# Kernel optimization log

Hardware: AMD Instinct MI355X
Metric: run time of the kernel (lower is better)

Reference implementation:

```python
import jax, jax.numpy as jnp
import numpy as np

HID = 128
OUT = 128
NC = 100000
NA = 1024
FC = 256
FA = 4096

def _sage(x_src, x_dst, ei, Wl, bl, Wr):
    # PyG SAGEConv, mean aggregation, bipartite:
    # out[i] = lin_l(mean_{j->i} x_src[j]) + lin_r(x_dst[i])
    n_dst = x_dst.shape[0]
    src, dst = ei[0], ei[1]
    msg = x_src[src]                                  # [E, F_src] gather
    agg = jax.ops.segment_sum(msg, dst, num_segments=n_dst)
    cnt = jax.ops.segment_sum(jnp.ones((ei.shape[1],), x_src.dtype), dst, num_segments=n_dst)
    mean = agg / jnp.clip(cnt, 1.0, None)[:, None]
    return mean @ Wl.T + bl + x_dst @ Wr.T

def setup_inputs() -> dict:
    key = jax.random.key(0)
    ks = jax.random.split(key, 20)
    d = {}
    d["article_x"] = jax.random.normal(ks[0], (1, FA), jnp.float32)
    d["community_x"] = jax.random.normal(ks[1], (NC, FC), jnp.float32)
    # bipartite edges: row = article node idx (<NA), col = community idx (<NC)
    d["e_wb"] = jnp.stack([jax.random.randint(ks[2], (500000,), 0, NA, jnp.int32),
                            jax.random.randint(ks[3], (500000,), 0, NC, jnp.int32)])
    d["e_mb"] = jnp.stack([jax.random.randint(ks[4], (500000,), 0, NA, jnp.int32),
                            jax.random.randint(ks[5], (500000,), 0, NC, jnp.int32)])
    d["e_cc"] = jax.random.randint(ks[6], (2, 800000), 0, NC, jnp.int32)
    s = lambda k, sh: jax.random.normal(k, sh, jnp.float32) * (1.0 / np.sqrt(sh[-1]))
    d["W_lin1"] = s(ks[7], (NA, FA)); d["b_lin1"] = jnp.zeros((NA,), jnp.float32)
    d["Wl1"] = s(ks[8], (HID, 1));   d["bl1"] = jnp.zeros((HID,), jnp.float32); d["Wr1"] = s(ks[9], (HID, FC))
    d["Wl2"] = s(ks[10], (HID, 1));  d["bl2"] = jnp.zeros((HID,), jnp.float32); d["Wr2"] = s(ks[11], (HID, HID))
    d["Wl3"] = s(ks[12], (HID, HID)); d["bl3"] = jnp.zeros((HID,), jnp.float32); d["Wr3"] = s(ks[13], (HID, FC))
    d["W_lin2"] = s(ks[14], (OUT, HID)); d["b_lin2"] = jnp.zeros((OUT,), jnp.float32)
    d["Wd1"] = s(ks[15], (OUT, 2 * OUT)); d["bd1"] = jnp.zeros((OUT,), jnp.float32)
    d["Wd2"] = s(ks[16], (1, OUT)); d["bd2"] = jnp.zeros((1,), jnp.float32)
    return d

def reference(article_x, community_x, e_wb, e_mb, e_cc,
              W_lin1, b_lin1, Wl1, bl1, Wr1, Wl2, bl2, Wr2,
              Wl3, bl3, Wr3, W_lin2, b_lin2, Wd1, bd1, Wd2, bd2):
    # encoder
    art = (article_x @ W_lin1.T + b_lin1).reshape(NA, 1)      # [1024, 1]
    h1 = jax.nn.relu(_sage(art, community_x, e_wb, Wl1, bl1, Wr1))   # [NC, HID]
    h2 = jax.nn.relu(_sage(art, h1, e_mb, Wl2, bl2, Wr2))            # [NC, HID]
    h3 = jax.nn.relu(_sage(h2, community_x, e_cc, Wl3, bl3, Wr3))    # [NC, HID]
    z = h3 @ W_lin2.T + b_lin2                                       # [NC, OUT]
    # edge decoder on interacts_with edges
    row, col = e_cc[0], e_cc[1]
    zz = jnp.concatenate([z[row], z[col]], axis=-1)                  # [E, 2*OUT]
    h = jax.nn.relu(zz @ Wd1.T + bd1)
    return (h @ Wd2.T + bd2).reshape(-1)                             # [E]
```

## Files before the change

kernel.cpp:

```cpp
#include <hip/hip_runtime.h>

#define NC 100000
#define NA 1024
#define FA 4096
#define MAXD 40

typedef _Float16 half8 __attribute__((ext_vector_type(8)));
typedef _Float16 half4v __attribute__((ext_vector_type(4)));
typedef _Float16 half2v __attribute__((ext_vector_type(2)));
typedef float floatx4 __attribute__((ext_vector_type(4)));

#define CNT_OFF 4294967296.0
#define CNT_INV 2.3283064365386963e-10

__device__ __forceinline__ void cvt_range(const float* __restrict__ in,
                                          _Float16* __restrict__ out, int n4,
                                          int bid, int nb) {
    int t = bid * 256 + threadIdx.x;
    int stride = nb * 256;
    for (int i = t; i < n4; i += stride) {
        float4 v = ((const float4*)in)[i];
        half4v h = {(_Float16)v.x, (_Float16)v.y, (_Float16)v.z, (_Float16)v.w};
        ((half4v*)out)[i] = h;
    }
}

__device__ __forceinline__ void edge_seg(const int* __restrict__ ei, int E,
                                         const float* __restrict__ art,
                                         double* __restrict__ acd, int bid, int nb) {
    int t = bid * 256 + threadIdx.x;
    int stride = nb * 256;
    for (int e = t; e < E; e += stride) {
        int s = ei[e], d = ei[E + e];
        atomicAdd(&acd[d], (double)art[s] + CNT_OFF);
    }
}

__device__ __forceinline__ void scat_seg(const int* __restrict__ ei, int E,
                                         int* __restrict__ cnt, int2* __restrict__ se2,
                                         int bid, int nb) {
    int t = bid * 256 + threadIdx.x;
    int stride = nb * 256;
    for (int e = t; e < E; e += stride) {
        int s = ei[e], d = ei[E + e];
        int pos = atomicAdd(&cnt[d], 1);
        if (pos < MAXD) se2[(size_t)d * MAXD + pos] = make_int2(s, e);
    }
}

__device__ __forceinline__ void wcomb_seg(const float* __restrict__ Wd1,
                                          const float* __restrict__ Wlin2,
                                          _Float16* __restrict__ Wuh,
                                          _Float16* __restrict__ Wvh, int bid) {
    int i = bid * 2 + (threadIdx.x >> 7);
    int j = threadIdx.x & 127;
    float au = 0.f, av = 0.f;
    for (int m = 0; m < 128; ++m) {
        float wl = Wlin2[m * 128 + j];
        au = fmaf(Wd1[i * 256 + m], wl, au);
        av = fmaf(Wd1[i * 256 + 128 + m], wl, av);
    }
    Wuh[i * 128 + j] = (_Float16)au;
    Wvh[i * 128 + j] = (_Float16)av;
}

__device__ __forceinline__ void bcomb_seg(const float* __restrict__ Wd1,
                                          const float* __restrict__ b2,
                                          const float* __restrict__ bd1,
                                          float* __restrict__ bu, float* __restrict__ bv) {
    int i = threadIdx.x;
    if (i >= 128) return;
    float su = 0.f, sv = 0.f;
    for (int m = 0; m < 128; ++m) {
        float b = b2[m];
        su = fmaf(Wd1[i * 256 + m], b, su);
        sv = fmaf(Wd1[i * 256 + 128 + m], b, sv);
    }
    bu[i] = su + bd1[i];
    bv[i] = sv;
}

#define ART_BLKS 256
#define Z1_BLKS  64
#define Z2_BLKS  16
__global__ void k_art(const float* __restrict__ ax, const float* __restrict__ W,
                      const float* __restrict__ b, float* __restrict__ art,
                      float4* __restrict__ zacd, float4* __restrict__ zcnt) {
    int blk = blockIdx.x;
    if (blk >= ART_BLKS) {
        blk -= ART_BLKS;
        float4 z = make_float4(0.f, 0.f, 0.f, 0.f);
        if (blk < Z1_BLKS) {
            int n4 = NC;
            int t = blk * 256 + threadIdx.x;
            for (int i = t; i < n4; i += Z1_BLKS * 256) zacd[i] = z;
        } else {
            blk -= Z1_BLKS;
            int n4 = NC / 4;
            int t = blk * 256 + threadIdx.x;
            for (int i = t; i < n4; i += Z2_BLKS * 256) zcnt[i] = z;
        }
        return;
    }
    int wave = (blk * 256 + threadIdx.x) >> 6;
    int lane = threadIdx.x & 63;
    if (wave >= NA) return;
    const float* wr = W + (size_t)wave * FA;
    float s = 0.f;
    #pragma unroll
    for (int i = 0; i < FA; i += 256) {
        float4 a  = *(const float4*)&ax[i + 4 * lane];
        float4 wv = *(const float4*)&wr[i + 4 * lane];
        s += a.x * wv.x + a.y * wv.y + a.z * wv.z + a.w * wv.w;
    }
    for (int off = 32; off; off >>= 1) s += __shfl_down(s, off);
    if (lane == 0) art[wave] = s + b[wave];
}

#define FRONT_WB   1024
#define FRONT_MB   1024
#define FRONT_SC   768
#define FRONT_WCVT 96
#define FRONT_WCOMB 64
#define FRONT_BCOMB 1
#define FRONT_CVT  8192
#define FRONT_TOTAL (FRONT_WB + FRONT_MB + FRONT_SC + FRONT_WCVT + FRONT_WCOMB + FRONT_BCOMB + FRONT_CVT)

__global__ __launch_bounds__(256)
void k_front(const int* __restrict__ e_wb, int E1,
             const int* __restrict__ e_mb, int E2,
             const int* __restrict__ e_cc, int E3,
             const float* __restrict__ art,
             double* __restrict__ acd1, double* __restrict__ acd2,
             int* __restrict__ cnt3, int2* __restrict__ se2,
             const float* __restrict__ Wr1, _Float16* __restrict__ Wr1h,
             const float* __restrict__ Wr2, _Float16* __restrict__ Wr2h,
             const float* __restrict__ Wl3, _Float16* __restrict__ Wl3h,
             const float* __restrict__ Wr3, _Float16* __restrict__ Wr3h,
             const float* __restrict__ Wd1, const float* __restrict__ Wlin2,
             _Float16* __restrict__ Wuh, _Float16* __restrict__ Wvh,
             const float* __restrict__ b2, const float* __restrict__ bd1,
             float* __restrict__ bu, float* __restrict__ bv,
             const float* __restrict__ cx, _Float16* __restrict__ cxh)
{
    int b = blockIdx.x;
    if (b < FRONT_WB) { edge_seg(e_wb, E1, art, acd1, b, FRONT_WB); return; }
    b -= FRONT_WB;
    if (b < FRONT_MB) { edge_seg(e_mb, E2, art, acd2, b, FRONT_MB); return; }
    b -= FRONT_MB;
    if (b < FRONT_SC) { scat_seg(e_cc, E3, cnt3, se2, b, FRONT_SC); return; }
    b -= FRONT_SC;
    if (b < FRONT_WCVT) {
        if (b < 32) cvt_range(Wr1, Wr1h, 8192, b, 32);
        else if (b < 48) cvt_range(Wr2, Wr2h, 4096, b - 32, 16);
        else if (b < 64) cvt_range(Wl3, Wl3h, 4096, b - 48, 16);
        else cvt_range(Wr3, Wr3h, 8192, b - 64, 32);
        return;
    }
    b -= FRONT_WCVT;
    if (b < FRONT_WCOMB) { wcomb_seg(Wd1, Wlin2, Wuh, Wvh, b); return; }
    b -= FRONT_WCOMB;
    if (b < FRONT_BCOMB) { bcomb_seg(Wd1, b2, bd1, bu, bv); return; }
    b -= FRONT_BCOMB;
    cvt_range(cx, cxh, NC * 64, b, FRONT_CVT);
}

__device__ __forceinline__ float mean_from_packed(double t) {
    double cd = rint(t * CNT_INV);
    float sum = (float)(t - cd * CNT_OFF);
    float cc = (float)cd;
    cc = cc > 1.f ? cc : 1.f;
    return sum / cc;
}

#define MID_GB  ((NC + 127) / 128)

__global__ __launch_bounds__(256)
void k_enc12(const _Float16* __restrict__ cxh, const _Float16* __restrict__ Wr1h,
             const _Float16* __restrict__ Wr2h,
             const float* __restrict__ bl1, const double* __restrict__ acd1,
             const float* __restrict__ Wl1,
             const float* __restrict__ bl2, const double* __restrict__ acd2,
             const float* __restrict__ Wl2,
             _Float16* __restrict__ out, int N)
{
    __shared__ _Float16 lds[128 * 40 + 128 * 136];
    _Float16* Bh  = lds;
    _Float16* Ah  = lds + 128 * 40;
    _Float16* h1t = lds + 128 * 40;

    const int t = threadIdx.x, lane = t & 63, w = t >> 6;
    const int rowbase = blockIdx.x * 128;
    const bool isA = t < 128;
    const int rr = isA ? t : t - 128;
    const int fr = lane & 15;
    const int kq = (lane >> 4) << 3;

    floatx4 zero4 = {0.f, 0.f, 0.f, 0.f};
    floatx4 acc[2][8];
    #pragma unroll
    for (int i = 0; i < 2; ++i)
        #pragma unroll
        for (int cf = 0; cf < 8; ++cf) acc[i][cf] = zero4;

    float4 p0, p1, p2, p3;
    float4 zf = make_float4(0.f, 0.f, 0.f, 0.f);
    {
        bool ok = true; const _Float16* base;
        if (isA) { int row = rowbase + rr; ok = row < N; base = ok ? &cxh[(size_t)row * 256] : Ah; }
        else base = &Wr1h[(size_t)rr * 256];
        const float4* s4 = (const float4*)base;
        p0 = ok ? s4[0] : zf; p1 = ok ? s4[1] : zf; p2 = ok ? s4[2] : zf; p3 = ok ? s4[3] : zf;
    }
    for (int tile = 0; tile < 8; ++tile) {
        float4* dst = (float4*)(isA ? &Ah[rr * 40] : &Bh[rr * 40]);
        dst[0] = p0; dst[1] = p1; dst[2] = p2; dst[3] = p3;
        __syncthreads();
        if (tile < 7) {
            int ko = (tile + 1) << 5;
            bool ok = true; const _Float16* base;
            if (isA) { int row = rowbase + rr; ok = row < N; base = ok ? &cxh[(size_t)row * 256 + ko] : Ah; }
            else base = &Wr1h[(size_t)rr * 256 + ko];
            const float4* s4 = (const float4*)base;
            p0 = ok ? s4[0] : zf; p1 = ok ? s4[1] : zf; p2 = ok ? s4[2] : zf; p3 = ok ? s4[3] : zf;
        }
        half8 af0 = *(const half8*)&Ah[(w * 32 + fr) * 40 + kq];
        half8 af1 = *(const half8*)&Ah[(w * 32 + 16 + fr) * 40 + kq];
        #pragma unroll
        for (int cf = 0; cf < 8; ++cf) {
            half8 bf = *(const half8*)&Bh[(cf * 16 + fr) * 40 + kq];
            acc[0][cf] = __builtin_amdgcn_mfma_f32_16x16x32_f16(af0, bf, acc[0][cf], 0, 0, 0);
            acc[1][cf] = __builtin_amdgcn_mfma_f32_16x16x32_f16(af1, bf, acc[1][cf], 0, 0, 0);
        }
        __syncthreads();
    }

    {
        float blc[8], wlc[8];
        #pragma unroll
        for (int cf = 0; cf < 8; ++cf) { int col = cf * 16 + fr; blc[cf] = bl1[col]; wlc[cf] = Wl1[col]; }
        #pragma unroll
        for (int i = 0; i < 2; ++i) {
            #pragma unroll
            for (int j = 0; j < 4; ++j) {
                int lrow = w * 32 + i * 16 + ((lane >> 4) << 2) + j;
                int grow = rowbase + lrow;
                float m = 0.f;
                if (grow < N) m = mean_from_packed(acd1[grow]);
                #pragma unroll
                for (int cf = 0; cf < 8; ++cf) {
                    float v = acc[i][cf][j] + blc[cf] + m * wlc[cf];
                    v = fmaxf(v, 0.f);
                    h1t[lrow * 136 + cf * 16 + fr] = (_Float16)v;
                }
            }
        }
    }
    __syncthreads();

    #pragma unroll
    for (int i = 0; i < 2; ++i)
        #pragma unroll
        for (int cf = 0; cf < 8; ++cf) acc[i][cf] = zero4;
    if (!isA) {
        const float4* s4 = (const float4*)&Wr2h[(size_t)rr * 128];
        p0 = s4[0]; p1 = s4[1]; p2 = s4[2]; p3 = s4[3];
    }
    for (int tt = 0; tt < 4; ++tt) {
        if (!isA) { float4* d = (float4*)&Bh[rr * 40]; d[0] = p0; d[1] = p1; d[2] = p2; d[3] = p3; }
        __syncthreads();
        if (!isA && tt < 3) {
            const float4* s4 = (const float4*)&Wr2h[(size_t)rr * 128 + ((tt + 1) << 5)];
            p0 = s4[0]; p1 = s4[1]; p2 = s4[2]; p3 = s4[3];
        }
        half8 af0 = *(const half8*)&h1t[(w * 32 + fr) * 136 + (tt << 5) + kq];
        half8 af1 = *(const half8*)&h1t[(w * 32 + 16 + fr) * 136 + (tt << 5) + kq];
        #pragma unroll
        for (int cf = 0; cf < 8; ++cf) {
            half8 bf = *(const half8*)&Bh[(cf * 16 + fr) * 40 + kq];
            acc[0][cf] = __builtin_amdgcn_mfma_f32_16x16x32_f16(af0, bf, acc[0][cf], 0, 0, 0);
            acc[1][cf] = __builtin_amdgcn_mfma_f32_16x16x32_f16(af1, bf, acc[1][cf], 0, 0, 0);
        }
        __syncthreads();
    }

    {
        float blc[8], wlc[8];
        #pragma unroll
        for (int cf = 0; cf < 8; ++cf) { int col = cf * 16 + fr; blc[cf] = bl2[col]; wlc[cf] = Wl2[col]; }
        #pragma unroll
        for (int i = 0; i < 2; ++i) {
            #pragma unroll
            for (int j = 0; j < 4; ++j) {
                int grow = rowbase + w * 32 + i * 16 + ((lane >> 4) << 2) + j;
                if (grow < N) {
                    float m = mean_from_packed(acd2[grow]);
                    #pragma unroll
                    for (int cf = 0; cf < 8; ++cf) {
                        float v = acc[i][cf][j] + blc[cf] + m * wlc[cf];
                        v = fmaxf(v, 0.f);
                        out[(size_t)grow * 128 + cf * 16 + fr] = (_Float16)v;
                    }
                }
            }
        }
    }
}

__global__ __launch_bounds__(256)
void k_csr_agg_h(const int* __restrict__ cnt3, const int2* __restrict__ se2,
                 const _Float16* __restrict__ h, _Float16* __restrict__ agg) {
    int node = (blockIdx.x * blockDim.x + threadIdx.x) >> 6;
    int lane = threadIdx.x & 63;
    if (node >= NC) return;
    int d = cnt3[node]; if (d > MAXD) d = MAXD;
    const int2* bucket = se2 + (size_t)node * MAXD;
    int sj = 0;
    if (lane < d) sj = bucket[lane].x;
    float sx = 0.f, sy = 0.f;
    #pragma unroll 4
    for (int j = 0; j < d; ++j) {
        int src = __shfl(sj, j);
        half2v m = *(const half2v*)&h[(size_t)src * 128 + 2 * lane];
        sx += (float)m[0]; sy += (float)m[1];
    }
    half2v r = {(_Float16)sx, (_Float16)sy};
    *(half2v*)&agg[(size_t)node * 128 + 2 * lane] = r;
}

__global__ __launch_bounds__(256)
void k_enc3uv(const _Float16* __restrict__ aggh, const _Float16* __restrict__ Wl3h,
              const _Float16* __restrict__ cxh, const _Float16* __restrict__ Wr3h,
              const float* __restrict__ bl3, const int* __restrict__ rcnt,
              const _Float16* __restrict__ Wuh, const float* __restrict__ bu,
              const _Float16* __restrict__ Wvh, const float* __restrict__ bv,
              _Float16* __restrict__ uout, _Float16* __restrict__ vout, int N)
{
    __shared__ _Float16 lds[128 * 40 + 128 * 136];
    _Float16* Bh  = lds;
    _Float16* Ah  = lds + 128 * 40;
    _Float16* h3t = lds + 128 * 40;

    const int t = threadIdx.x, lane = t & 63, w = t >> 6;
    const int rowbase = blockIdx.x * 128;
    const bool isA = t < 128;
    const int rr = isA ? t : t - 128;
    const int fr = lane & 15;
    const int kq = (lane >> 4) << 3;

    floatx4 zero4 = {0.f, 0.f, 0.f, 0.f};
    floatx4 acc[2][8];
    #pragma unroll
    for (int i = 0; i < 2; ++i)
        #pragma unroll
        for (int cf = 0; cf < 8; ++cf) acc[i][cf] = zero4;

    float4 p0, p1, p2, p3;
    float4 zf = make_float4(0.f, 0.f, 0.f, 0.f);
    {
        bool ok = true; const _Float16* base;
        if (isA) { int row = rowbase + rr; ok = row < N; base = ok ? &aggh[(size_t)row * 128] : Ah; }
        else base = &Wl3h[(size_t)rr * 128];
        const float4* s4 = (const float4*)base;
        p0 = ok ? s4[0] : zf; p1 = ok ? s4[1] : zf; p2 = ok ? s4[2] : zf; p3 = ok ? s4[3] : zf;
    }
    for (int tile = 0; tile < 12; ++tile) {
        float4* dst = (float4*)(isA ? &Ah[rr * 40] : &Bh[rr * 40]);
        dst[0] = p0; dst[1] = p1; dst[2] = p2; dst[3] = p3;
        __syncthreads();
        if (tile < 11) {
            int tn = tile + 1;
            bool ok = true; const _Float16* base;
            if (tn < 4) {
                int ko = tn << 5;
                if (isA) { int row = rowbase + rr; ok = row < N; base = ok ? &aggh[(size_t)row * 128 + ko] : Ah; }
                else base = &Wl3h[(size_t)rr * 128 + ko];
            } else {
                int ko = (tn - 4) << 5;
                if (isA) { int row = rowbase + rr; ok = row < N; base = ok ? &cxh[(size_t)row * 256 + ko] : Ah; }
                else base = &Wr3h[(size_t)rr * 256 + ko];
            }
            const float4* s4 = (const float4*)base;
            p0 = ok ? s4[0] : zf; p1 = ok ? s4[1] : zf; p2 = ok ? s4[2] : zf; p3 = ok ? s4[3] : zf;
        }
        half8 af0 = *(const half8*)&Ah[(w * 32 + fr) * 40 + kq];
        half8 af1 = *(const half8*)&Ah[(w * 32 + 16 + fr) * 40 + kq];
        #pragma unroll
        for (int cf = 0; cf < 8; ++cf) {
            half8 bf = *(const half8*)&Bh[(cf * 16 + fr) * 40 + kq];
            acc[0][cf] = __builtin_amdgcn_mfma_f32_16x16x32_f16(af0, bf, acc[0][cf], 0, 0, 0);
            acc[1][cf] = __builtin_amdgcn_mfma_f32_16x16x32_f16(af1, bf, acc[1][cf], 0, 0, 0);
        }
        if (tile == 3) {
            #pragma unroll
            for (int i = 0; i < 2; ++i)
                #pragma unroll
                for (int j = 0; j < 4; ++j) {
                    int row = rowbase + w * 32 + i * 16 + ((lane >> 4) << 2) + j;
                    float c = (row < N) ? (float)rcnt[row] : 1.f;
                    c = c > 1.f ? c : 1.f;
                    float inv = 1.f / c;
                    #pragma unroll
                    for (int cf = 0; cf < 8; ++cf) acc[i][cf][j] *= inv;
                }
        }
        __syncthreads();
    }

    {
        float blc[8];
        #pragma unroll
        for (int cf = 0; cf < 8; ++cf) blc[cf] = bl3[cf * 16 + fr];
        #pragma unroll
        for (int i = 0; i < 2; ++i) {
            #pragma unroll
            for (int j = 0; j < 4; ++j) {
                int lrow = w * 32 + i * 16 + ((lane >> 4) << 2) + j;
                #pragma unroll
                for (int cf = 0; cf < 8; ++cf) {
                    float v = acc[i][cf][j] + blc[cf];
                    v = fmaxf(v, 0.f);
                    h3t[lrow * 136 + cf * 16 + fr] = (_Float16)v;
                }
            }
        }
    }
    __syncthreads();

    for (int ph = 0; ph < 2; ++ph) {
        const _Float16* Wp = ph ? Wvh : Wuh;
        const float* bp = ph ? bv : bu;
        _Float16* op = ph ? vout : uout;
        #pragma unroll
        for (int i = 0; i < 2; ++i)
            #pragma unroll
            for (int cf = 0; cf < 8; ++cf) acc[i][cf] = zero4;
        if (!isA) {
            const float4* s4 = (const float4*)&Wp[(size_t)rr * 128];
            p0 = s4[0]; p1 = s4[1]; p2 = s4[2]; p3 = s4[3];
        }
        for (int tt = 0; tt < 4; ++tt) {
            if (!isA) { float4* d = (float4*)&Bh[rr * 40]; d[0] = p0; d[1] = p1; d[2] = p2; d[3] = p3; }
            __syncthreads();
            if (!isA && tt < 3) {
                const float4* s4 = (const float4*)&Wp[(size_t)rr * 128 + ((tt + 1) << 5)];
                p0 = s4[0]; p1 = s4[1]; p2 = s4[2]; p3 = s4[3];
            }
            half8 af0 = *(const half8*)&h3t[(w * 32 + fr) * 136 + (tt << 5) + kq];
            half8 af1 = *(const half8*)&h3t[(w * 32 + 16 + fr) * 136 + (tt << 5) + kq];
            #pragma unroll
            for (int cf = 0; cf < 8; ++cf) {
                half8 bf = *(const half8*)&Bh[(cf * 16 + fr) * 40 + kq];
                acc[0][cf] = __builtin_amdgcn_mfma_f32_16x16x32_f16(af0, bf, acc[0][cf], 0, 0, 0);
                acc[1][cf] = __builtin_amdgcn_mfma_f32_16x16x32_f16(af1, bf, acc[1][cf], 0, 0, 0);
            }
            __syncthreads();
        }
        float bc[8];
        #pragma unroll
        for (int cf = 0; cf < 8; ++cf) bc[cf] = bp[cf * 16 + fr];
        #pragma unroll
        for (int i = 0; i < 2; ++i) {
            #pragma unroll
            for (int j = 0; j < 4; ++j) {
                int grow = rowbase + w * 32 + i * 16 + ((lane >> 4) << 2) + j;
                if (grow < N) {
                    #pragma unroll
                    for (int cf = 0; cf < 8; ++cf)
                        op[(size_t)grow * 128 + cf * 16 + fr] = (_Float16)(acc[i][cf][j] + bc[cf]);
                }
            }
        }
    }
}

__global__ __launch_bounds__(256)
void k_decoder_h(const int* __restrict__ cnt3, const int2* __restrict__ se2,
                 const _Float16* __restrict__ u, const _Float16* __restrict__ v,
                 const float* __restrict__ wd2, const float* __restrict__ bd2,
                 float* __restrict__ out) {
    int node = (blockIdx.x * blockDim.x + threadIdx.x) >> 6;
    if (node >= NC) return;
    int lane = threadIdx.x & 63;
    int g = lane >> 3, s = lane & 7;

    float wf[16], vf[16];
    #pragma unroll
    for (int q = 0; q < 16; ++q) wf[q] = wd2[s * 16 + q];
    {
        half8 va = *(const half8*)&v[(size_t)node * 128 + s * 16];
        half8 vb = *(const half8*)&v[(size_t)node * 128 + s * 16 + 8];
        #pragma unroll
        for (int q = 0; q < 8; ++q) { vf[q] = (float)va[q]; vf[8 + q] = (float)vb[q]; }
    }
    float bb = bd2[0];

    int d = cnt3[node]; if (d > MAXD) d = MAXD;
    const int2* bucket = se2 + (size_t)node * MAXD;
    int sj = 0, ej = 0;
    if (lane < d) { int2 p = bucket[lane]; sj = p.x; ej = p.y; }

    for (int jb = 0; jb < d; jb += 8) {
        int j = jb + g;
        float p = 0.f;
        bool act = j < d;
        int src = __shfl(sj, j);
        int eid = __shfl(ej, j);
        if (act) {
            half8 ua = *(const half8*)&u[(size_t)src * 128 + s * 16];
            half8 ub = *(const half8*)&u[(size_t)src * 128 + s * 16 + 8];
            #pragma unroll
            for (int q = 0; q < 8; ++q) {
                p = fmaf(wf[q],     fmaxf((float)ua[q] + vf[q],     0.f), p);
                p = fmaf(wf[8 + q], fmaxf((float)ub[q] + vf[8 + q], 0.f), p);
            }
        }
        p += __shfl_xor(p, 1);
        p += __shfl_xor(p, 2);
        p += __shfl_xor(p, 4);
        if (act && s == 0) out[eid] = p + bb;
    }
}

extern "C" void kernel_launch(void* const* d_in, const int* in_sizes, int n_in,
                              void* d_out, int out_size, void* d_ws, size_t ws_size,
                              hipStream_t stream) {
    const float* article_x = (const float*)d_in[0];
    const float* cx     = (const float*)d_in[1];
    const int*   e_wb   = (const int*)d_in[2];
    const int*   e_mb   = (const int*)d_in[3];
    const int*   e_cc   = (const int*)d_in[4];
    const float* W_lin1 = (const float*)d_in[5];
    const float* b_lin1 = (const float*)d_in[6];
    const float* Wl1    = (const float*)d_in[7];
    const float* bl1    = (const float*)d_in[8];
    const float* Wr1    = (const float*)d_in[9];
    const float* Wl2    = (const float*)d_in[10];
    const float* bl2    = (const float*)d_in[11];
    const float* Wr2    = (const float*)d_in[12];
    const float* Wl3    = (const float*)d_in[13];
    const float* bl3    = (const float*)d_in[14];
    const float* Wr3    = (const float*)d_in[15];
    const float* W_lin2 = (const float*)d_in[16];
    const float* b_lin2 = (const float*)d_in[17];
    const float* Wd1    = (const float*)d_in[18];
    const float* bd1    = (const float*)d_in[19];
    const float* Wd2    = (const float*)d_in[20];
    const float* bd2    = (const float*)d_in[21];
    float* out = (float*)d_out;

    const int E1 = in_sizes[2] / 2;
    const int E2 = in_sizes[3] / 2;
    const int E3 = in_sizes[4] / 2;

    double* acd1 = (double*)d_ws;
    double* acd2 = acd1 + NC;
    float* ws = (float*)(acd2 + NC);
    size_t o = 0;
    float* art   = ws;      o += 1024;
    float* buf   = ws + o;  o += 128;
    float* bvf   = ws + o;  o += 128;
    int* cnt3   = (int*)(ws + o); o += NC;
    int2* se2   = (int2*)(ws + o); o += (size_t)2 * NC * MAXD;
    _Float16* hws = (_Float16*)(ws + o);
    size_t ho = 0;
    _Float16* cxh    = hws + ho; ho += (size_t)NC * 256;
    _Float16* B1h    = hws + ho; ho += (size_t)NC * 128;
    _Float16* B2h    = hws + ho; ho += (size_t)NC * 128;
    _Float16* Wr1h   = hws + ho; ho += 128 * 256;
    _Float16* Wr2h   = hws + ho; ho += 128 * 128;
    _Float16* Wl3h   = hws + ho; ho += 128 * 128;
    _Float16* Wr3h   = hws + ho; ho += 128 * 256;
    _Float16* Wuh    = hws + ho; ho += 128 * 128;
    _Float16* Wvh    = hws + ho; ho += 128 * 128;

    k_art<<<ART_BLKS + Z1_BLKS + Z2_BLKS, 256, 0, stream>>>(
        article_x, W_lin1, b_lin1, art, (float4*)acd1, (float4*)cnt3);

    k_front<<<FRONT_TOTAL, 256, 0, stream>>>(
        e_wb, E1, e_mb, E2, e_cc, E3, art, acd1, acd2, cnt3, se2,
        Wr1, Wr1h, Wr2, Wr2h, Wl3, Wl3h, Wr3, Wr3h,
        Wd1, W_lin2, Wuh, Wvh, b_lin2, bd1, buf, bvf, cx, cxh);

    k_enc12<<<MID_GB, 256, 0, stream>>>(
        cxh, Wr1h, Wr2h, bl1, acd1, Wl1, bl2, acd2, Wl2, B1h, NC);

    const int GW = (NC * 64 + 255) / 256;
    k_csr_agg_h<<<GW, 256, 0, stream>>>(cnt3, se2, B1h, B2h);
    k_enc3uv<<<MID_GB, 256, 0, stream>>>(B2h, Wl3h, cxh, Wr3h,
                                         bl3, cnt3, Wuh, buf, Wvh, bvf,
                                         B1h, B2h, NC);
    k_decoder_h<<<GW, 256, 0, stream>>>(cnt3, se2, B1h, B2h, Wd2, bd2, out);
}
```

Measured before the change: 317.8 us.

## Move e_cc CSR bucket scatter from front kernel into encoder-12 kernel

The atomic bucket scatter of the interacts_with edges is moved out of the front kernel and given its own block range inside a merged mid kernel that also runs the layer-1/2 encoder GEMM. The scatter only has to finish before the CSR aggregation kernel, so it can now overlap with the MFMA-heavy encoder blocks instead of competing with the other atomic segments in the front kernel. The scatter blocks now allocate the encoder's shared-memory array even though they don't use it, which may limit how many of them are resident at once, and the scatter runs with fewer blocks than before.

```diff
diff --git a/kernel.cpp b/kernel.cpp
--- a/kernel.cpp
+++ b/kernel.cpp
@@ -33,18 +33,6 @@
     for (int e = t; e < E; e += stride) {
         int s = ei[e], d = ei[E + e];
         atomicAdd(&acd[d], (double)art[s] + CNT_OFF);
-    }
-}
-
-__device__ __forceinline__ void scat_seg(const int* __restrict__ ei, int E,
-                                         int* __restrict__ cnt, int2* __restrict__ se2,
-                                         int bid, int nb) {
-    int t = bid * 256 + threadIdx.x;
-    int stride = nb * 256;
-    for (int e = t; e < E; e += stride) {
-        int s = ei[e], d = ei[E + e];
-        int pos = atomicAdd(&cnt[d], 1);
-        if (pos < MAXD) se2[(size_t)d * MAXD + pos] = make_int2(s, e);
     }
 }
 
@@ -119,20 +107,17 @@
 
 #define FRONT_WB   1024
 #define FRONT_MB   1024
-#define FRONT_SC   768
 #define FRONT_WCVT 96
 #define FRONT_WCOMB 64
 #define FRONT_BCOMB 1
 #define FRONT_CVT  8192
-#define FRONT_TOTAL (FRONT_WB + FRONT_MB + FRONT_SC + FRONT_WCVT + FRONT_WCOMB + FRONT_BCOMB + FRONT_CVT)
+#define FRONT_TOTAL (FRONT_WB + FRONT_MB + FRONT_WCVT + FRONT_WCOMB + FRONT_BCOMB + FRONT_CVT)
 
 __global__ __launch_bounds__(256)
 void k_front(const int* __restrict__ e_wb, int E1,
              const int* __restrict__ e_mb, int E2,
-             const int* __restrict__ e_cc, int E3,
              const float* __restrict__ art,
              double* __restrict__ acd1, double* __restrict__ acd2,
-             int* __restrict__ cnt3, int2* __restrict__ se2,
              const float* __restrict__ Wr1, _Float16* __restrict__ Wr1h,
              const float* __restrict__ Wr2, _Float16* __restrict__ Wr2h,
              const float* __restrict__ Wl3, _Float16* __restrict__ Wl3h,
@@ -148,8 +133,6 @@
     b -= FRONT_WB;
     if (b < FRONT_MB) { edge_seg(e_mb, E2, art, acd2, b, FRONT_MB); return; }
     b -= FRONT_MB;
-    if (b < FRONT_SC) { scat_seg(e_cc, E3, cnt3, se2, b, FRONT_SC); return; }
-    b -= FRONT_SC;
     if (b < FRONT_WCVT) {
         if (b < 32) cvt_range(Wr1, Wr1h, 8192, b, 32);
         else if (b < 48) cvt_range(Wr2, Wr2h, 4096, b - 32, 16);
@@ -173,24 +156,22 @@
     return sum / cc;
 }
 
-#define MID_GB  ((NC + 127) / 128)
-
-__global__ __launch_bounds__(256)
-void k_enc12(const _Float16* __restrict__ cxh, const _Float16* __restrict__ Wr1h,
-             const _Float16* __restrict__ Wr2h,
-             const float* __restrict__ bl1, const double* __restrict__ acd1,
-             const float* __restrict__ Wl1,
-             const float* __restrict__ bl2, const double* __restrict__ acd2,
-             const float* __restrict__ Wl2,
-             _Float16* __restrict__ out, int N)
+__device__ __forceinline__
+void enc12_body(_Float16* lds, int blk,
+                const _Float16* __restrict__ cxh, const _Float16* __restrict__ Wr1h,
+                const _Float16* __restrict__ Wr2h,
+                const float* __restrict__ bl1, const double* __restrict__ acd1,
+                const float* __restrict__ Wl1,
+                const float* __restrict__ bl2, const double* __restrict__ acd2,
+                const float* __restrict__ Wl2,
+                _Float16* __restrict__ out, int N)
 {
-    __shared__ _Float16 lds[128 * 40 + 128 * 136];
     _Float16* Bh  = lds;
     _Float16* Ah  = lds + 128 * 40;
     _Float16* h1t = lds + 128 * 40;
 
     const int t = threadIdx.x, lane = t & 63, w = t >> 6;
-    const int rowbase = blockIdx.x * 128;
+    const int rowbase = blk * 128;
     const bool isA = t < 128;
     const int rr = isA ? t : t - 128;
     const int fr = lane & 15;
@@ -305,6 +286,35 @@
             }
         }
     }
+}
+
+#define MID_SC  256
+#define MID_GB  ((NC + 127) / 128)
+
+__global__ __launch_bounds__(256)
+void k_mid(const _Float16* __restrict__ cxh, const _Float16* __restrict__ Wr1h,
+           const _Float16* __restrict__ Wr2h,
+           const float* __restrict__ bl1, const double* __restrict__ acd1,
+           const float* __restrict__ Wl1,
+           const float* __restrict__ bl2, const double* __restrict__ acd2,
+           const float* __restrict__ Wl2,
+           _Float16* __restrict__ out, int N,
+           const int* __restrict__ e_cc, int E3,
+           int* __restrict__ cnt3, int2* __restrict__ se2)
+{
+    __shared__ _Float16 lds[128 * 40 + 128 * 136];
+    if (blockIdx.x < MID_SC) {
+        int t = blockIdx.x * 256 + threadIdx.x;
+        int stride = MID_SC * 256;
+        #pragma unroll 4
+        for (int e = t; e < E3; e += stride) {
+            int s = e_cc[e], d = e_cc[E3 + e];
+            int pos = atomicAdd(&cnt3[d], 1);
+            if (pos < MAXD) se2[(size_t)d * MAXD + pos] = make_int2(s, e);
+        }
+        return;
+    }
+    enc12_body(lds, blockIdx.x - MID_SC, cxh, Wr1h, Wr2h, bl1, acd1, Wl1, bl2, acd2, Wl2, out, N);
 }
 
 __global__ __launch_bounds__(256)
@@ -578,12 +588,13 @@
         article_x, W_lin1, b_lin1, art, (float4*)acd1, (float4*)cnt3);
 
     k_front<<<FRONT_TOTAL, 256, 0, stream>>>(
-        e_wb, E1, e_mb, E2, e_cc, E3, art, acd1, acd2, cnt3, se2,
+        e_wb, E1, e_mb, E2, art, acd1, acd2,
         Wr1, Wr1h, Wr2, Wr2h, Wl3, Wl3h, Wr3, Wr3h,
         Wd1, W_lin2, Wuh, Wvh, b_lin2, bd1, buf, bvf, cx, cxh);
 
-    k_enc12<<<MID_GB, 256, 0, stream>>>(
-        cxh, Wr1h, Wr2h, bl1, acd1, Wl1, bl2, acd2, Wl2, B1h, NC);
+    k_mid<<<MID_SC + MID_GB, 256, 0, stream>>>(
+        cxh, Wr1h, Wr2h, bl1, acd1, Wl1, bl2, acd2, Wl2,
+        B1h, NC, e_cc, E3, cnt3, se2);
 
     const int GW = (NC * 64 + 255) / 256;
     k_csr_agg_h<<<GW, 256, 0, stream>>>(cnt3, se2, B1h, B2h);
```

New measurement: 314.3 us. Within noise of the previous version (-1.1%).
